# Kernel optimization log

Measured on AMD Instinct MI355X. Metric: run time of the kernel, lower is better.

Reference implementation:

```python
import jax, jax.numpy as jnp
import numpy as np

B, T, C, N = 8, 2048, 512, 1024  # batch, num_tokens, num_features, num_nodes


def setup_inputs() -> dict:
    key = jax.random.key(0)
    ks = jax.random.split(key, 8)
    s_q = 1.0 / np.sqrt(T)
    s_c = 1.0 / np.sqrt(C)
    return {
        "x": jax.random.normal(ks[0], (B, T, C), dtype=jnp.float32),
        "Wq": jax.random.uniform(ks[1], (N, T), jnp.float32, -s_q, s_q),
        "bq": jax.random.uniform(ks[2], (N,), jnp.float32, -s_q, s_q),
        "Wk": jax.random.uniform(ks[3], (C, C), jnp.float32, -s_c, s_c),
        "Wv": jax.random.uniform(ks[4], (C, C), jnp.float32, -s_c, s_c),
        "Wout": jax.random.uniform(ks[5], (C, C), jnp.float32, -s_c, s_c),
        "bout": jax.random.uniform(ks[6], (C,), jnp.float32, -s_c, s_c),
    }


def reference(x, Wq, bq, Wk, Wv, Wout, bout):
    scale = C ** (-0.5)
    # to_q applied along the token axis: q[b,n,c] = sum_t x[b,t,c] * Wq[n,t] + bq[n]
    q = jnp.einsum('btc,nt->bnc', x, Wq) + bq[None, :, None]
    k = jnp.einsum('btc,dc->btd', x, Wk)   # [B,T,C]
    v = jnp.einsum('btc,dc->btd', x, Wv)   # [B,T,C]
    sim = jnp.einsum('bnc,btc->bnt', q, k) * scale  # [B,N,T]
    # winner-take-all over the node axis (dim=1): keep only per-token max rows
    amax = jnp.max(sim, axis=1, keepdims=True)      # [B,1,T]
    mask = sim < amax                                # True -> suppressed
    big_neg = -jnp.finfo(sim.dtype).max
    sim = jnp.where(mask, big_neg, sim)
    sim = sim - jnp.max(sim, axis=-1, keepdims=True)
    att = jax.nn.softmax(sim, axis=-1)
    att = jnp.where(mask, 0.0, att)                  # [B,N,T]
    out = jnp.einsum('bnt,btc->bnc', att, v)         # [B,N,C]
    out = jnp.einsum('bnc,dc->bnd', out, Wout) + bout
    return (out, att)
```

## Files before the change

kernel.cpp:

```cpp
#include <hip/hip_runtime.h>
#include <hip/hip_bf16.h>
#include <cfloat>

#define BB 8
#define TT 2048
#define CC 512
#define NNODE 1024

#define GAP_MARGIN 2e-4f
#define MAXC 6
#define NSLOT 512

typedef float f32x4 __attribute__((ext_vector_type(4)));
typedef short bf16x8 __attribute__((ext_vector_type(8)));
typedef float float4v __attribute__((ext_vector_type(4)));
typedef unsigned short u16x4 __attribute__((ext_vector_type(4)));
typedef unsigned short u16x8 __attribute__((ext_vector_type(8)));

__device__ __forceinline__ unsigned fkey(float v) {
  unsigned u = __float_as_uint(v);
  return (u & 0x80000000u) ? ~u : (u | 0x80000000u);
}
__device__ __forceinline__ float fdec(unsigned k) {
  unsigned u = (k & 0x80000000u) ? (k & 0x7FFFFFFFu) : ~k;
  return __uint_as_float(u);
}
__device__ __forceinline__ unsigned short bf16_rn(float f) {
  unsigned u = __float_as_uint(f);
  u += 0x7FFFu + ((u >> 16) & 1u);
  return (unsigned short)(u >> 16);
}
__device__ __forceinline__ float bf16_tof(unsigned short h) {
  return __uint_as_float(((unsigned)h) << 16);
}

__global__ __launch_bounds__(256) void split2_kernel(
    const float* __restrict__ src, unsigned short* __restrict__ hi,
    unsigned short* __restrict__ lo, long long n4) {
  long long i = (long long)blockIdx.x * 256 + threadIdx.x;
  long long stride = (long long)gridDim.x * 256;
  for (; i < n4; i += stride) {
    float4v v = ((const float4v*)src)[i];
    u16x4 h, l;
#pragma unroll
    for (int j = 0; j < 4; ++j) {
      unsigned short hh = bf16_rn(v[j]);
      h[j] = hh;
      l[j] = bf16_rn(v[j] - bf16_tof(hh));
    }
    ((u16x4*)hi)[i] = h;
    ((u16x4*)lo)[i] = l;
  }
}

__global__ __launch_bounds__(256) void split1_kernel(
    const float* __restrict__ src, unsigned short* __restrict__ hi, long long n4) {
  long long i = (long long)blockIdx.x * 256 + threadIdx.x;
  long long stride = (long long)gridDim.x * 256;
  for (; i < n4; i += stride) {
    float4v v = ((const float4v*)src)[i];
    u16x4 h;
#pragma unroll
    for (int j = 0; j < 4; ++j) h[j] = bf16_rn(v[j]);
    ((u16x4*)hi)[i] = h;
  }
}

__global__ __launch_bounds__(256) void mfma_q(
    const unsigned short* __restrict__ Wqh, const unsigned short* __restrict__ Wql,
    const unsigned short* __restrict__ xh, const unsigned short* __restrict__ xl,
    const float* __restrict__ bq,
    unsigned short* __restrict__ qh, unsigned short* __restrict__ ql) {
  __shared__ unsigned short Ah[128][40], Al[128][40], Bh[64][40], Bl[64][40];

  const int b = blockIdx.z;
  const unsigned short* xhb = xh + (size_t)b * TT * CC;
  const unsigned short* xlb = xl + (size_t)b * TT * CC;
  const int m0 = blockIdx.y * 128;
  const int n0 = blockIdx.x * 64;
  const int tid = threadIdx.x;
  const int l = tid & 63;
  const int wid = tid >> 6;
  const int wy = wid >> 1;
  const int wx = wid & 1;
  const int lrow = l & 15, lkb = (l >> 4) * 8;
  const int nn = tid & 63, kq = tid >> 6;

  f32x4 acc[4][2] = {};

  for (int k0 = 0; k0 < TT; k0 += 32) {
#pragma unroll
    for (int p = 0; p < 2; ++p) {
      int idx = tid + p * 256;
      int ar = idx >> 2, ack = (idx & 3) * 8;
      *(u16x8*)&Ah[ar][ack] = *(const u16x8*)(Wqh + (size_t)(m0 + ar) * TT + k0 + ack);
      *(u16x8*)&Al[ar][ack] = *(const u16x8*)(Wql + (size_t)(m0 + ar) * TT + k0 + ack);
    }
    {
      u16x8 hv, lv;
#pragma unroll
      for (int j = 0; j < 8; ++j) {
        size_t gi = (size_t)(k0 + kq * 8 + j) * CC + n0 + nn;
        hv[j] = xhb[gi];
        lv[j] = xlb[gi];
      }
      *(u16x8*)&Bh[nn][kq * 8] = hv;
      *(u16x8*)&Bl[nn][kq * 8] = lv;
    }
    __syncthreads();

    bf16x8 ah[4], al[4], bh[2], bl[2];
#pragma unroll
    for (int mf = 0; mf < 4; ++mf) {
      ah[mf] = *(const bf16x8*)&Ah[wy * 64 + mf * 16 + lrow][lkb];
      al[mf] = *(const bf16x8*)&Al[wy * 64 + mf * 16 + lrow][lkb];
    }
#pragma unroll
    for (int nf = 0; nf < 2; ++nf) {
      bh[nf] = *(const bf16x8*)&Bh[wx * 32 + nf * 16 + lrow][lkb];
      bl[nf] = *(const bf16x8*)&Bl[wx * 32 + nf * 16 + lrow][lkb];
    }
#pragma unroll
    for (int mf = 0; mf < 4; ++mf)
#pragma unroll
      for (int nf = 0; nf < 2; ++nf) {
        acc[mf][nf] =
            __builtin_amdgcn_mfma_f32_16x16x32_bf16(ah[mf], bh[nf], acc[mf][nf], 0, 0, 0);
        acc[mf][nf] =
            __builtin_amdgcn_mfma_f32_16x16x32_bf16(ah[mf], bl[nf], acc[mf][nf], 0, 0, 0);
        acc[mf][nf] =
            __builtin_amdgcn_mfma_f32_16x16x32_bf16(al[mf], bh[nf], acc[mf][nf], 0, 0, 0);
      }
    __syncthreads();
  }

#pragma unroll
  for (int mf = 0; mf < 4; ++mf)
#pragma unroll
    for (int r = 0; r < 4; ++r) {
      int m = m0 + wy * 64 + mf * 16 + (l >> 4) * 4 + r;
      float bias = bq[m];
#pragma unroll
      for (int nf = 0; nf < 2; ++nf) {
        int n = n0 + wx * 32 + nf * 16 + lrow;
        float v = acc[mf][nf][r] + bias;
        size_t off = ((size_t)b * NNODE + m) * CC + n;
        unsigned short h = bf16_rn(v);
        qh[off] = h;
        ql[off] = bf16_rn(v - bf16_tof(h));
      }
    }
}

__global__ __launch_bounds__(256) void mfma_kv_pre(
    const unsigned short* __restrict__ xh, const unsigned short* __restrict__ xl,
    const unsigned short* __restrict__ Wkh, const unsigned short* __restrict__ Wkl,
    const unsigned short* __restrict__ Wvh,
    unsigned short* __restrict__ kh, unsigned short* __restrict__ kl,
    unsigned short* __restrict__ vout) {
  __shared__ unsigned short Ah[64][40], Al[64][40], Bkh[128][40], Bkl[128][40],
      Bvh[128][40];

  const int b = blockIdx.z;
  const unsigned short* xhb = xh + (size_t)b * TT * CC;
  const unsigned short* xlb = xl + (size_t)b * TT * CC;
  const int m0 = blockIdx.y * 64;
  const int n0 = blockIdx.x * 128;
  const int tid = threadIdx.x;
  const int l = tid & 63;
  const int wid = tid >> 6;
  const int wy = wid >> 1, wx = wid & 1;
  const int lrow = l & 15, lkb = (l >> 4) * 8;
  const int rr = tid >> 2, cq = tid & 3;

  f32x4 acck[2][4] = {}, accv[2][4] = {};

  for (int k0 = 0; k0 < CC; k0 += 32) {
    *(u16x8*)&Ah[rr][cq * 8] = *(const u16x8*)(xhb + (size_t)(m0 + rr) * CC + k0 + cq * 8);
    *(u16x8*)&Al[rr][cq * 8] = *(const u16x8*)(xlb + (size_t)(m0 + rr) * CC + k0 + cq * 8);
#pragma unroll
    for (int p = 0; p < 2; ++p) {
      int idx = tid + p * 256;
      int r = idx >> 2, ck = (idx & 3) * 8;
      *(u16x8*)&Bkh[r][ck] = *(const u16x8*)(Wkh + (size_t)(n0 + r) * CC + k0 + ck);
      *(u16x8*)&Bkl[r][ck] = *(const u16x8*)(Wkl + (size_t)(n0 + r) * CC + k0 + ck);
      *(u16x8*)&Bvh[r][ck] = *(const u16x8*)(Wvh + (size_t)(n0 + r) * CC + k0 + ck);
    }
    __syncthreads();

    bf16x8 ah[2], al[2], bkh4[4], bkl4[4], bvh4[4];
#pragma unroll
    for (int mf = 0; mf < 2; ++mf) {
      ah[mf] = *(const bf16x8*)&Ah[wy * 32 + mf * 16 + lrow][lkb];
      al[mf] = *(const bf16x8*)&Al[wy * 32 + mf * 16 + lrow][lkb];
    }
#pragma unroll
    for (int nf = 0; nf < 4; ++nf) {
      bkh4[nf] = *(const bf16x8*)&Bkh[wx * 64 + nf * 16 + lrow][lkb];
      bkl4[nf] = *(const bf16x8*)&Bkl[wx * 64 + nf * 16 + lrow][lkb];
      bvh4[nf] = *(const bf16x8*)&Bvh[wx * 64 + nf * 16 + lrow][lkb];
    }
#pragma unroll
    for (int mf = 0; mf < 2; ++mf)
#pragma unroll
      for (int nf = 0; nf < 4; ++nf) {
        acck[mf][nf] =
            __builtin_amdgcn_mfma_f32_16x16x32_bf16(ah[mf], bkh4[nf], acck[mf][nf], 0, 0, 0);
        acck[mf][nf] =
            __builtin_amdgcn_mfma_f32_16x16x32_bf16(ah[mf], bkl4[nf], acck[mf][nf], 0, 0, 0);
        acck[mf][nf] =
            __builtin_amdgcn_mfma_f32_16x16x32_bf16(al[mf], bkh4[nf], acck[mf][nf], 0, 0, 0);
        accv[mf][nf] =
            __builtin_amdgcn_mfma_f32_16x16x32_bf16(ah[mf], bvh4[nf], accv[mf][nf], 0, 0, 0);
      }
    __syncthreads();
  }

#pragma unroll
  for (int mf = 0; mf < 2; ++mf)
#pragma unroll
    for (int r = 0; r < 4; ++r) {
      int m = m0 + wy * 32 + mf * 16 + (l >> 4) * 4 + r;
#pragma unroll
      for (int nf = 0; nf < 4; ++nf) {
        int n = n0 + wx * 64 + nf * 16 + lrow;
        size_t off = ((size_t)b * TT + m) * CC + n;
        float kvv = acck[mf][nf][r];
        unsigned short h = bf16_rn(kvv);
        kh[off] = h;
        kl[off] = bf16_rn(kvv - bf16_tof(h));
        vout[off] = bf16_rn(accv[mf][nf][r]);
      }
    }
}

__global__ __launch_bounds__(256) void mfma_sim_pre(
    const unsigned short* __restrict__ qh, const unsigned short* __restrict__ ql,
    const unsigned short* __restrict__ kh, const unsigned short* __restrict__ kl,
    unsigned long long* __restrict__ cand1, unsigned long long* __restrict__ cand2,
    unsigned long long* __restrict__ cand3) {
  __shared__ unsigned short Ah[128][40], Al[128][40], Bh[64][40], Bl[64][40];
  __shared__ unsigned long long c1[64], c2[64], c3[64];

  const int b = blockIdx.z;
  const unsigned short* qhb = qh + (size_t)b * NNODE * CC;
  const unsigned short* qlb = ql + (size_t)b * NNODE * CC;
  const unsigned short* khb = kh + (size_t)b * TT * CC;
  const unsigned short* klb = kl + (size_t)b * TT * CC;
  const int n0 = blockIdx.y * 128;
  const int t0 = blockIdx.x * 64;
  const int tid = threadIdx.x;
  const int l = tid & 63;
  const int wid = tid >> 6;
  const int wy = wid >> 1, wx = wid & 1;
  const int lrow = l & 15, lkb = (l >> 4) * 8;
  const int br = tid >> 2, bck = (tid & 3) * 8;

  if (tid < 64) { c1[tid] = 0ULL; c2[tid] = 0ULL; c3[tid] = 0ULL; }

  f32x4 acc[4][2] = {};

  for (int k0 = 0; k0 < CC; k0 += 32) {
#pragma unroll
    for (int p = 0; p < 2; ++p) {
      int idx = tid + p * 256;
      int r = idx >> 2, ck = (idx & 3) * 8;
      *(u16x8*)&Ah[r][ck] = *(const u16x8*)(qhb + (size_t)(n0 + r) * CC + k0 + ck);
      *(u16x8*)&Al[r][ck] = *(const u16x8*)(qlb + (size_t)(n0 + r) * CC + k0 + ck);
    }
    if (br < 64) {
      *(u16x8*)&Bh[br][bck] = *(const u16x8*)(khb + (size_t)(t0 + br) * CC + k0 + bck);
      *(u16x8*)&Bl[br][bck] = *(const u16x8*)(klb + (size_t)(t0 + br) * CC + k0 + bck);
    }
    __syncthreads();

    bf16x8 ah[4], al[4], bh[2], bl[2];
#pragma unroll
    for (int mf = 0; mf < 4; ++mf) {
      ah[mf] = *(const bf16x8*)&Ah[wy * 64 + mf * 16 + lrow][lkb];
      al[mf] = *(const bf16x8*)&Al[wy * 64 + mf * 16 + lrow][lkb];
    }
#pragma unroll
    for (int nf = 0; nf < 2; ++nf) {
      bh[nf] = *(const bf16x8*)&Bh[wx * 32 + nf * 16 + lrow][lkb];
      bl[nf] = *(const bf16x8*)&Bl[wx * 32 + nf * 16 + lrow][lkb];
    }
#pragma unroll
    for (int mf = 0; mf < 4; ++mf)
#pragma unroll
      for (int nf = 0; nf < 2; ++nf) {
        acc[mf][nf] =
            __builtin_amdgcn_mfma_f32_16x16x32_bf16(ah[mf], bh[nf], acc[mf][nf], 0, 0, 0);
        acc[mf][nf] =
            __builtin_amdgcn_mfma_f32_16x16x32_bf16(ah[mf], bl[nf], acc[mf][nf], 0, 0, 0);
        acc[mf][nf] =
            __builtin_amdgcn_mfma_f32_16x16x32_bf16(al[mf], bh[nf], acc[mf][nf], 0, 0, 0);
      }
    __syncthreads();
  }

  const float scl = 0.04419417382415922f;
#pragma unroll
  for (int nf = 0; nf < 2; ++nf) {
    int tcol = wx * 32 + nf * 16 + lrow;
    unsigned long long m = 0ULL;
#pragma unroll
    for (int mf = 0; mf < 4; ++mf)
#pragma unroll
      for (int r = 0; r < 4; ++r) {
        unsigned node = (unsigned)(n0 + wy * 64 + mf * 16 + (l >> 4) * 4 + r);
        unsigned long long pk =
            ((unsigned long long)fkey(acc[mf][nf][r] * scl) << 32) | node;
        if (pk > m) m = pk;
      }
    atomicMax(&c1[tcol], m);
  }
  __syncthreads();
#pragma unroll
  for (int nf = 0; nf < 2; ++nf) {
    int tcol = wx * 32 + nf * 16 + lrow;
    unsigned w1 = (unsigned)c1[tcol];
    unsigned long long m = 0ULL;
#pragma unroll
    for (int mf = 0; mf < 4; ++mf)
#pragma unroll
      for (int r = 0; r < 4; ++r) {
        unsigned node = (unsigned)(n0 + wy * 64 + mf * 16 + (l >> 4) * 4 + r);
        if (node == w1) continue;
        unsigned long long pk =
            ((unsigned long long)fkey(acc[mf][nf][r] * scl) << 32) | node;
        if (pk > m) m = pk;
      }
    if (m) atomicMax(&c2[tcol], m);
  }
  __syncthreads();
#pragma unroll
  for (int nf = 0; nf < 2; ++nf) {
    int tcol = wx * 32 + nf * 16 + lrow;
    unsigned w1 = (unsigned)c1[tcol];
    unsigned w2 = (unsigned)c2[tcol];
    unsigned long long m = 0ULL;
#pragma unroll
    for (int mf = 0; mf < 4; ++mf)
#pragma unroll
      for (int r = 0; r < 4; ++r) {
        unsigned node = (unsigned)(n0 + wy * 64 + mf * 16 + (l >> 4) * 4 + r);
        if (node == w1 || node == w2) continue;
        unsigned long long pk =
            ((unsigned long long)fkey(acc[mf][nf][r] * scl) << 32) | node;
        if (pk > m) m = pk;
      }
    if (m) atomicMax(&c3[tcol], m);
  }
  __syncthreads();
  if (tid < 64) {
    size_t base = ((size_t)b * TT + (t0 + tid)) * 8 + blockIdx.y;
    cand1[base] = c1[tid];
    cand2[base] = c2[tid];
    cand3[base] = c3[tid];
  }
}

__global__ __launch_bounds__(256) void mfma_wout(
    const float* __restrict__ A, const float* __restrict__ Bm,
    float* __restrict__ Cp, const float* __restrict__ bias) {
  __shared__ unsigned short Ah[64][40], Bh[64][40];
  const int m0 = blockIdx.y * 64;
  const int n0 = blockIdx.x * 64;
  const int tid = threadIdx.x;
  const int l = tid & 63;
  const int wid = tid >> 6;
  const int wy = wid >> 1, wx = wid & 1;
  const int lrow = l & 15, lkb = (l >> 4) * 8;

  f32x4 acc[2][2] = {};

  for (int k0 = 0; k0 < CC; k0 += 32) {
#pragma unroll
    for (int p = 0; p < 2; ++p) {
      int idx = tid + p * 256;
      int r = idx >> 3, c = (idx & 7) * 4;
      float4v va = *(const float4v*)(A + (size_t)(m0 + r) * CC + k0 + c);
      float4v vb = *(const float4v*)(Bm + (size_t)(n0 + r) * CC + k0 + c);
#pragma unroll
      for (int i = 0; i < 4; ++i) {
        Ah[r][c + i] = bf16_rn(va[i]);
        Bh[r][c + i] = bf16_rn(vb[i]);
      }
    }
    __syncthreads();

    bf16x8 ah[2], bh[2];
#pragma unroll
    for (int mf = 0; mf < 2; ++mf)
      ah[mf] = *(const bf16x8*)&Ah[wy * 32 + mf * 16 + lrow][lkb];
#pragma unroll
    for (int nf = 0; nf < 2; ++nf)
      bh[nf] = *(const bf16x8*)&Bh[wx * 32 + nf * 16 + lrow][lkb];
#pragma unroll
    for (int mf = 0; mf < 2; ++mf)
#pragma unroll
      for (int nf = 0; nf < 2; ++nf)
        acc[mf][nf] =
            __builtin_amdgcn_mfma_f32_16x16x32_bf16(ah[mf], bh[nf], acc[mf][nf], 0, 0, 0);
    __syncthreads();
  }

#pragma unroll
  for (int mf = 0; mf < 2; ++mf)
#pragma unroll
    for (int r = 0; r < 4; ++r) {
      int m = m0 + wy * 32 + mf * 16 + (l >> 4) * 4 + r;
#pragma unroll
      for (int nf = 0; nf < 2; ++nf) {
        int n = n0 + wx * 32 + nf * 16 + lrow;
        Cp[(size_t)m * CC + n] = acc[mf][nf][r] + bias[n];
      }
    }
}

__global__ __launch_bounds__(256) void fill_zero(unsigned* __restrict__ p, long long n) {
  long long i = (long long)blockIdx.x * 256 + threadIdx.x;
  long long stride = (long long)gridDim.x * 256;
  for (; i < n; i += stride) p[i] = 0u;
}

__global__ __launch_bounds__(256) void transpose_kernel(
    const float* __restrict__ src, float* __restrict__ dst, int R, int C) {
  __shared__ float tile[32][33];
  int r0 = blockIdx.y * 32, c0 = blockIdx.x * 32;
  int tx = threadIdx.x & 31, ty = threadIdx.x >> 5;
#pragma unroll
  for (int i = 0; i < 4; ++i)
    tile[ty + i * 8][tx] = src[(size_t)(r0 + ty + i * 8) * C + c0 + tx];
  __syncthreads();
#pragma unroll
  for (int i = 0; i < 4; ++i)
    dst[(size_t)(c0 + ty + i * 8) * R + r0 + tx] = tile[tx][ty + i * 8];
}

__global__ __launch_bounds__(256) void merge_flag_kernel(
    const unsigned long long* __restrict__ cand1,
    const unsigned long long* __restrict__ cand2,
    const unsigned long long* __restrict__ cand3,
    unsigned long long* __restrict__ amaxIdx,
    unsigned* __restrict__ gcount, unsigned* __restrict__ gflag,
    unsigned* __restrict__ clist) {
  int bt = blockIdx.x * 256 + threadIdx.x;
  unsigned long long best = 0ULL;
#pragma unroll
  for (int nb = 0; nb < 8; ++nb) {
    unsigned long long v = cand1[(size_t)bt * 8 + nb];
    if (v > best) best = v;
  }
  amaxIdx[bt] = best;
  float v1 = fdec((unsigned)(best >> 32));
  float thr = v1 - GAP_MARGIN;
  unsigned bestnode = (unsigned)best;

  unsigned nodes[MAXC];
  int cnt = 0;
#pragma unroll
  for (int nb = 0; nb < 8; ++nb) {
    unsigned long long cs[3] = {cand1[(size_t)bt * 8 + nb], cand2[(size_t)bt * 8 + nb],
                                cand3[(size_t)bt * 8 + nb]};
#pragma unroll
    for (int s = 0; s < 3; ++s) {
      float v = fdec((unsigned)(cs[s] >> 32));
      unsigned nd = (unsigned)cs[s];
      if (v >= thr && nd != bestnode && cnt < MAXC) nodes[cnt++] = nd;
    }
  }
  if (cnt > 0) {
    unsigned p = atomicAdd(gcount, 1u);
    if (p < NSLOT) {
      gflag[p] = (unsigned)bt;
      clist[(size_t)bt * 8] = (unsigned)(cnt + 1);
      clist[(size_t)bt * 8 + 1] = bestnode;
      for (int i = 0; i < cnt; ++i) clist[(size_t)bt * 8 + 2 + i] = nodes[i];
    }
  }
}

__global__ __launch_bounds__(256) void recheck_k64(
    const float* __restrict__ x, const float* __restrict__ WkT,
    const unsigned* __restrict__ gcount, const unsigned* __restrict__ gflag,
    double* __restrict__ k64g) {
  __shared__ float xs[CC];
  __shared__ double kpart[64][4];

  const unsigned cnt = min(*gcount, (unsigned)NSLOT);
  const int slot = blockIdx.x >> 3;
  const int dchunk = blockIdx.x & 7;
  if ((unsigned)slot >= cnt) return;
  const int tid = threadIdx.x;

  unsigned bt = gflag[slot];
  int b = bt >> 11, t = bt & (TT - 1);
  const float* xr = x + ((size_t)b * TT + t) * CC;
  xs[tid] = xr[tid];
  xs[tid + 256] = xr[tid + 256];
  __syncthreads();

  const int d = dchunk * 64 + (tid & 63);
  const int part = tid >> 6;
  const int cbase = part * 128;
  double a0 = 0.0, a1 = 0.0;
#pragma unroll 8
  for (int i = 0; i < 64; ++i) {
    int c = cbase + 2 * i;
    a0 = fma((double)WkT[(size_t)c * CC + d], (double)xs[c], a0);
    a1 = fma((double)WkT[(size_t)(c + 1) * CC + d], (double)xs[c + 1], a1);
  }
  kpart[tid & 63][part] = a0 + a1;
  __syncthreads();
  if (tid < 64) {
    double s = (kpart[tid][0] + kpart[tid][1]) + (kpart[tid][2] + kpart[tid][3]);
    k64g[(size_t)slot * CC + dchunk * 64 + tid] = s;
  }
}

__global__ __launch_bounds__(256) void recheck_z(
    const float* __restrict__ x, const unsigned* __restrict__ gcount,
    const unsigned* __restrict__ gflag, const double* __restrict__ k64g,
    float* __restrict__ zg) {
  __shared__ float tile[64][129];
  __shared__ double k64l[CC];
  __shared__ double zp[64][4];

  const unsigned cnt = min(*gcount, (unsigned)NSLOT);
  const int slot = blockIdx.x >> 5;
  const int tchunk = blockIdx.x & 31;
  if ((unsigned)slot >= cnt) return;
  const int tid = threadIdx.x;

  unsigned bt = gflag[slot];
  int b = bt >> 11;
  const float* xb = x + (size_t)b * TT * CC;
  const int tok0 = tchunk * 64;

  k64l[tid] = k64g[(size_t)slot * CC + tid];
  k64l[tid + 256] = k64g[(size_t)slot * CC + tid + 256];

  const int tok = tid >> 2;
  const int part = tid & 3;
  double z0 = 0.0, z1 = 0.0;

  for (int p = 0; p < 4; ++p) {
    __syncthreads();
    int c0 = p * 128;
#pragma unroll
    for (int j = 0; j < 32; ++j) {
      int lin = j * 256 + tid;
      int r = lin >> 7, col = lin & 127;
      tile[r][col] = xb[(size_t)(tok0 + r) * CC + c0 + col];
    }
    __syncthreads();
#pragma unroll
    for (int i = 0; i < 16; ++i) {
      int cl = part * 32 + 2 * i;
      z0 = fma((double)tile[tok][cl], k64l[c0 + cl], z0);
      z1 = fma((double)tile[tok][cl + 1], k64l[c0 + cl + 1], z1);
    }
  }
  zp[tok][part] = z0 + z1;
  __syncthreads();
  if (tid < 64) {
    double z = (zp[tid][0] + zp[tid][1]) + (zp[tid][2] + zp[tid][3]);
    zg[(size_t)slot * TT + tok0 + tid] = (float)z;
  }
}

__global__ __launch_bounds__(256) void recheck_cand(
    const float* __restrict__ Wq, const float* __restrict__ bq,
    const unsigned* __restrict__ gcount, const unsigned* __restrict__ gflag,
    const unsigned* __restrict__ clist, const double* __restrict__ k64g,
    const float* __restrict__ zg, unsigned long long* __restrict__ amaxIdx) {
  __shared__ double red[4];
  __shared__ double ssumS;

  const unsigned cnt = min(*gcount, (unsigned)NSLOT);
  const int slot = blockIdx.x;
  if ((unsigned)slot >= cnt) return;
  const int tid = threadIdx.x;

  unsigned bt = gflag[slot];

  double ps = k64g[(size_t)slot * CC + tid] + k64g[(size_t)slot * CC + tid + 256];
#pragma unroll
  for (int off = 32; off > 0; off >>= 1) ps += __shfl_down(ps, off, 64);
  if ((tid & 63) == 0) red[tid >> 6] = ps;
  __syncthreads();
  if (tid == 0) ssumS = (red[0] + red[1]) + (red[2] + red[3]);
  __syncthreads();
  const double ssum = ssumS;

  const double scl = 0.04419417382415922;
  unsigned ncand = clist[(size_t)bt * 8];
  unsigned long long bestpk = 0ULL;
  double bestv = -1e300;
  for (unsigned ci = 0; ci < ncand; ++ci) {
    unsigned n = clist[(size_t)bt * 8 + 1 + ci];
    const float* wq = Wq + (size_t)n * TT;
    const float* zr = zg + (size_t)slot * TT;
    double a = 0.0;
#pragma unroll
    for (int i = 0; i < TT / 256; ++i) {
      int tp = tid + i * 256;
      a = fma((double)wq[tp], (double)zr[tp], a);
    }
#pragma unroll
    for (int off = 32; off > 0; off >>= 1) a += __shfl_down(a, off, 64);
    if ((tid & 63) == 0) red[tid >> 6] = a;
    __syncthreads();
    double s = ((red[0] + red[1]) + (red[2] + red[3])) + (double)bq[n] * ssum;
    if (s > bestv) {
      bestv = s;
      bestpk = ((unsigned long long)fkey((float)(s * scl)) << 32) | n;
    }
    __syncthreads();
  }
  if (tid == 0) amaxIdx[bt] = bestpk;
}

__global__ __launch_bounds__(256) void node_max_kernel(
    const unsigned long long* __restrict__ amaxIdx, unsigned* __restrict__ Mpack) {
  int i = blockIdx.x * 256 + threadIdx.x;
  unsigned long long pk = amaxIdx[i];
  int b = i >> 11;
  unsigned w = (unsigned)pk;
  atomicMax(&Mpack[b * NNODE + w], (unsigned)(pk >> 32));
}

__global__ __launch_bounds__(256) void node_denom_kernel(
    const unsigned long long* __restrict__ amaxIdx, const unsigned* __restrict__ Mpack,
    float* __restrict__ D, float* __restrict__ att_val) {
  int i = blockIdx.x * 256 + threadIdx.x;
  unsigned long long pk = amaxIdx[i];
  int b = i >> 11;
  unsigned w = (unsigned)pk;
  float amaxf = fdec((unsigned)(pk >> 32));
  float Mf = fdec(Mpack[b * NNODE + w]);
  float e = expf(amaxf - Mf);
  att_val[i] = e;
  atomicAdd(&D[b * NNODE + w], e);
}

__global__ __launch_bounds__(256) void att_write_kernel(
    const unsigned long long* __restrict__ amaxIdx, const float* __restrict__ D,
    float* __restrict__ att_val, float* __restrict__ att_out) {
  int i = blockIdx.x * 256 + threadIdx.x;
  unsigned long long pk = amaxIdx[i];
  int b = i >> 11;
  int t = i & (TT - 1);
  unsigned w = (unsigned)pk;
  float a = att_val[i] / D[b * NNODE + w];
  att_val[i] = a;
  att_out[((size_t)b * NNODE + w) * TT + t] = a;
}

__global__ __launch_bounds__(256) void pv_scatter_kernel(
    const unsigned long long* __restrict__ amaxIdx, const float* __restrict__ att_val,
    const unsigned short* __restrict__ v, float* __restrict__ out0) {
  int bt = blockIdx.x;
  int b = bt >> 11;
  float a = att_val[bt];
  unsigned w = (unsigned)amaxIdx[bt];
  const unsigned short* vr = v + (size_t)bt * CC;
  float* orow = out0 + ((size_t)b * NNODE + w) * CC;
  for (int c = threadIdx.x; c < CC; c += 256)
    atomicAdd(&orow[c], a * bf16_tof(vr[c]));
}

extern "C" void kernel_launch(void* const* d_in, const int* in_sizes, int n_in,
                              void* d_out, int out_size, void* d_ws, size_t ws_size,
                              hipStream_t stream) {
  const float* x = (const float*)d_in[0];
  const float* Wq = (const float*)d_in[1];
  const float* bq = (const float*)d_in[2];
  const float* Wk = (const float*)d_in[3];
  const float* Wv = (const float*)d_in[4];
  const float* Wout = (const float*)d_in[5];
  const float* bout = (const float*)d_in[6];

  float* out = (float*)d_out;
  float* att_out = out + (size_t)BB * NNODE * CC;

  const size_t BNC = (size_t)BB * NNODE * CC;
  const size_t BTC = (size_t)BB * TT * CC;
  const size_t NT = (size_t)NNODE * TT;
  const size_t CC2 = (size_t)CC * CC;
  const size_t BT = (size_t)BB * TT;

  unsigned short* qh = (unsigned short*)d_ws;
  unsigned short* ql = qh + BNC;
  unsigned short* kh = ql + BNC;
  unsigned short* kl = kh + BTC;
  unsigned short* vbuf = kl + BTC;
  unsigned short* Wqh = vbuf + BTC;
  unsigned short* Wql = Wqh + NT;
  unsigned short* Wkh = Wql + NT;
  unsigned short* Wkl = Wkh + CC2;
  unsigned short* Wvh = Wkl + CC2;
  unsigned short* xh = Wvh + CC2;
  unsigned short* xl = xh + BTC;
  unsigned long long* amaxIdx = (unsigned long long*)(xl + BTC);
  unsigned* Mpack = (unsigned*)(amaxIdx + BT);
  float* D = (float*)(Mpack + (size_t)BB * NNODE);
  unsigned* gcount = (unsigned*)(D + (size_t)BB * NNODE);
  float* att_val = (float*)(gcount + 16);
  unsigned* gflag = (unsigned*)(att_val + BT);
  unsigned* clist = gflag + BT;
  float* out0 = (float*)xh;
  unsigned long long* cand1 = (unsigned long long*)(out0 + BNC);
  unsigned long long* cand2 = cand1 + BT * 8;
  unsigned long long* cand3 = cand2 + BT * 8;
  float* WkT = (float*)(cand3 + BT * 8);
  double* k64g = (double*)(WkT + CC2);
  float* zg = (float*)(k64g + (size_t)NSLOT * CC);

  dim3 blk(256);

  split2_kernel<<<dim3(2048), blk, 0, stream>>>(x, xh, xl, (long long)(BTC / 4));
  split2_kernel<<<dim3(1024), blk, 0, stream>>>(Wq, Wqh, Wql, (long long)(NT / 4));
  split2_kernel<<<dim3(256), blk, 0, stream>>>(Wk, Wkh, Wkl, (long long)(CC2 / 4));
  split1_kernel<<<dim3(256), blk, 0, stream>>>(Wv, Wvh, (long long)(CC2 / 4));

  fill_zero<<<dim3(64), blk, 0, stream>>>(Mpack, (long long)BB * NNODE * 2 + 16);
  fill_zero<<<dim3(4096), blk, 0, stream>>>((unsigned*)att_out,
                                            (long long)BB * NNODE * TT);

  mfma_q<<<dim3(CC / 64, NNODE / 128, BB), blk, 0, stream>>>(
      Wqh, Wql, xh, xl, bq, qh, ql);

  mfma_kv_pre<<<dim3(CC / 128, TT / 64, BB), blk, 0, stream>>>(
      xh, xl, Wkh, Wkl, Wvh, kh, kl, vbuf);

  transpose_kernel<<<dim3(CC / 32, CC / 32), blk, 0, stream>>>(Wk, WkT, CC, CC);

  mfma_sim_pre<<<dim3(TT / 64, NNODE / 128, BB), blk, 0, stream>>>(
      qh, ql, kh, kl, cand1, cand2, cand3);

  merge_flag_kernel<<<dim3(BB * TT / 256), blk, 0, stream>>>(
      cand1, cand2, cand3, amaxIdx, gcount, gflag, clist);

  recheck_k64<<<dim3(NSLOT * 8), blk, 0, stream>>>(x, WkT, gcount, gflag, k64g);
  recheck_z<<<dim3(NSLOT * 32), blk, 0, stream>>>(x, gcount, gflag, k64g, zg);
  recheck_cand<<<dim3(NSLOT), blk, 0, stream>>>(Wq, bq, gcount, gflag, clist,
                                                k64g, zg, amaxIdx);

  fill_zero<<<dim3(2048), blk, 0, stream>>>((unsigned*)out0, (long long)BB * NNODE * CC);

  node_max_kernel<<<dim3(BB * TT / 256), blk, 0, stream>>>(amaxIdx, Mpack);
  node_denom_kernel<<<dim3(BB * TT / 256), blk, 0, stream>>>(amaxIdx, Mpack, D, att_val);
  att_write_kernel<<<dim3(BB * TT / 256), blk, 0, stream>>>(amaxIdx, D, att_val, att_out);

  pv_scatter_kernel<<<dim3(BB * TT), blk, 0, stream>>>(amaxIdx, att_val, vbuf, out0);

  mfma_wout<<<dim3(CC / 64, BB * NNODE / 64), blk, 0, stream>>>(
      out0, Wout, out, bout);
}
```

Measured before the change: 370.3 us.

## Split-K the Q projection GEMM with larger N tiles and a reduction pass

```diff
diff --git a/kernel.cpp b/kernel.cpp
--- a/kernel.cpp
+++ b/kernel.cpp
@@ -66,29 +66,30 @@
   }
 }
 
-__global__ __launch_bounds__(256) void mfma_q(
+__global__ __launch_bounds__(256) void mfma_q_part(
     const unsigned short* __restrict__ Wqh, const unsigned short* __restrict__ Wql,
     const unsigned short* __restrict__ xh, const unsigned short* __restrict__ xl,
-    const float* __restrict__ bq,
-    unsigned short* __restrict__ qh, unsigned short* __restrict__ ql) {
-  __shared__ unsigned short Ah[128][40], Al[128][40], Bh[64][40], Bl[64][40];
+    float* __restrict__ p0, float* __restrict__ p1) {
+  __shared__ unsigned short Ah[128][40], Al[128][40], Bh[128][40], Bl[128][40];
 
   const int b = blockIdx.z;
   const unsigned short* xhb = xh + (size_t)b * TT * CC;
   const unsigned short* xlb = xl + (size_t)b * TT * CC;
+  const int cb = blockIdx.x & 3;
+  const int kp = blockIdx.x >> 2;
   const int m0 = blockIdx.y * 128;
-  const int n0 = blockIdx.x * 64;
+  const int n0 = cb * 128;
+  float* dst = kp ? p1 : p0;
   const int tid = threadIdx.x;
   const int l = tid & 63;
   const int wid = tid >> 6;
-  const int wy = wid >> 1;
-  const int wx = wid & 1;
+  const int wy = wid >> 1, wx = wid & 1;
   const int lrow = l & 15, lkb = (l >> 4) * 8;
-  const int nn = tid & 63, kq = tid >> 6;
-
-  f32x4 acc[4][2] = {};
-
-  for (int k0 = 0; k0 < TT; k0 += 32) {
+
+  f32x4 acc[4][4] = {};
+
+  const int kbeg = kp * (TT / 2), kend = kbeg + (TT / 2);
+  for (int k0 = kbeg; k0 < kend; k0 += 32) {
 #pragma unroll
     for (int p = 0; p < 2; ++p) {
       int idx = tid + p * 256;
@@ -96,7 +97,10 @@
       *(u16x8*)&Ah[ar][ack] = *(const u16x8*)(Wqh + (size_t)(m0 + ar) * TT + k0 + ack);
       *(u16x8*)&Al[ar][ack] = *(const u16x8*)(Wql + (size_t)(m0 + ar) * TT + k0 + ack);
     }
-    {
+#pragma unroll
+    for (int p = 0; p < 2; ++p) {
+      int idx = tid + p * 256;
+      int nn = idx & 127, kq = idx >> 7;
       u16x8 hv, lv;
 #pragma unroll
       for (int j = 0; j < 8; ++j) {
@@ -109,21 +113,21 @@
     }
     __syncthreads();
 
-    bf16x8 ah[4], al[4], bh[2], bl[2];
+    bf16x8 ah[4], al[4], bh[4], bl[4];
 #pragma unroll
     for (int mf = 0; mf < 4; ++mf) {
       ah[mf] = *(const bf16x8*)&Ah[wy * 64 + mf * 16 + lrow][lkb];
       al[mf] = *(const bf16x8*)&Al[wy * 64 + mf * 16 + lrow][lkb];
     }
 #pragma unroll
-    for (int nf = 0; nf < 2; ++nf) {
-      bh[nf] = *(const bf16x8*)&Bh[wx * 32 + nf * 16 + lrow][lkb];
-      bl[nf] = *(const bf16x8*)&Bl[wx * 32 + nf * 16 + lrow][lkb];
+    for (int nf = 0; nf < 4; ++nf) {
+      bh[nf] = *(const bf16x8*)&Bh[wx * 64 + nf * 16 + lrow][lkb];
+      bl[nf] = *(const bf16x8*)&Bl[wx * 64 + nf * 16 + lrow][lkb];
     }
 #pragma unroll
     for (int mf = 0; mf < 4; ++mf)
 #pragma unroll
-      for (int nf = 0; nf < 2; ++nf) {
+      for (int nf = 0; nf < 4; ++nf) {
         acc[mf][nf] =
             __builtin_amdgcn_mfma_f32_16x16x32_bf16(ah[mf], bh[nf], acc[mf][nf], 0, 0, 0);
         acc[mf][nf] =
@@ -139,17 +143,24 @@
 #pragma unroll
     for (int r = 0; r < 4; ++r) {
       int m = m0 + wy * 64 + mf * 16 + (l >> 4) * 4 + r;
-      float bias = bq[m];
-#pragma unroll
-      for (int nf = 0; nf < 2; ++nf) {
-        int n = n0 + wx * 32 + nf * 16 + lrow;
-        float v = acc[mf][nf][r] + bias;
-        size_t off = ((size_t)b * NNODE + m) * CC + n;
-        unsigned short h = bf16_rn(v);
-        qh[off] = h;
-        ql[off] = bf16_rn(v - bf16_tof(h));
-      }
-    }
+#pragma unroll
+      for (int nf = 0; nf < 4; ++nf) {
+        int n = n0 + wx * 64 + nf * 16 + lrow;
+        dst[((size_t)b * NNODE + m) * CC + n] = acc[mf][nf][r];
+      }
+    }
+}
+
+__global__ __launch_bounds__(256) void qadd_kernel(
+    const float* __restrict__ p0, const float* __restrict__ p1,
+    const float* __restrict__ bq,
+    unsigned short* __restrict__ qh, unsigned short* __restrict__ ql) {
+  size_t i = (size_t)blockIdx.x * 256 + threadIdx.x;
+  int m = (int)((i / CC) & (NNODE - 1));
+  float v = p0[i] + p1[i] + bq[m];
+  unsigned short h = bf16_rn(v);
+  qh[i] = h;
+  ql[i] = bf16_rn(v - bf16_tof(h));
 }
 
 __global__ __launch_bounds__(256) void mfma_kv_pre(
@@ -718,6 +729,8 @@
   float* WkT = (float*)(cand3 + BT * 8);
   double* k64g = (double*)(WkT + CC2);
   float* zg = (float*)(k64g + (size_t)NSLOT * CC);
+  float* qp0 = (float*)kh;
+  float* qp1 = (float*)kl;
 
   dim3 blk(256);
 
@@ -730,8 +743,10 @@
   fill_zero<<<dim3(4096), blk, 0, stream>>>((unsigned*)att_out,
                                             (long long)BB * NNODE * TT);
 
-  mfma_q<<<dim3(CC / 64, NNODE / 128, BB), blk, 0, stream>>>(
-      Wqh, Wql, xh, xl, bq, qh, ql);
+  mfma_q_part<<<dim3(8, NNODE / 128, BB), blk, 0, stream>>>(
+      Wqh, Wql, xh, xl, qp0, qp1);
+  qadd_kernel<<<dim3((unsigned)(BNC / 256)), blk, 0, stream>>>(
+      qp0, qp1, bq, qh, ql);
 
   mfma_kv_pre<<<dim3(CC / 128, TT / 64, BB), blk, 0, stream>>>(
       xh, xl, Wkh, Wkl, Wvh, kh, kl, vbuf);
```

Measured after the change: 365.7 us. No clear change (-1.2%).
